# Kernel optimization log

Measured on AMD Instinct MI355X. Metric: run time of the kernel, lower is better.

Reference implementation:

```python
import jax, jax.numpy as jnp
import numpy as np

N_NODES = 100000
N_EDGES = 3200000
IN_DIM = 64
HID = 64


def setup_inputs() -> dict:
    key = jax.random.key(0)
    ks = jax.random.split(key, 12)
    x = jax.random.normal(ks[0], (N_NODES, IN_DIM), dtype=jnp.float32)
    edge_index = jax.random.randint(ks[1], (2, N_EDGES), 0, N_NODES, dtype=jnp.int64)
    tau = jax.random.uniform(ks[2], (N_NODES, 1), dtype=jnp.float32)
    d1 = IN_DIM + 1  # augmented feature dim
    s1 = 1.0 / np.sqrt(d1)
    s2 = 1.0 / np.sqrt(HID)
    # SAGEConv: out = lin_l(mean_aggr) + lin_r(x); bias lives in lin_l. Weights stored [in, out].
    W1l = jax.random.uniform(ks[3], (d1, HID), jnp.float32, -s1, s1)
    b1l = jax.random.uniform(ks[4], (HID,), jnp.float32, -s1, s1)
    W1r = jax.random.uniform(ks[5], (d1, HID), jnp.float32, -s1, s1)
    W2l = jax.random.uniform(ks[6], (HID, HID), jnp.float32, -s2, s2)
    b2l = jax.random.uniform(ks[7], (HID,), jnp.float32, -s2, s2)
    W2r = jax.random.uniform(ks[8], (HID, HID), jnp.float32, -s2, s2)
    Wfc = jax.random.uniform(ks[9], (HID, 1), jnp.float32, -s2, s2)
    bfc = jax.random.uniform(ks[10], (1,), jnp.float32, -s2, s2)
    return {"x": x, "edge_index": edge_index, "tau": tau,
            "W1l": W1l, "b1l": b1l, "W1r": W1r,
            "W2l": W2l, "b2l": b2l, "W2r": W2r,
            "Wfc": Wfc, "bfc": bfc}


def _sage_conv(x, src, dst, Wl, bl, Wr, n_nodes):
    # mean aggregation of source-node features onto target nodes
    summed = jax.ops.segment_sum(x[src], dst, num_segments=n_nodes)  # [N, d]
    deg = jax.ops.segment_sum(jnp.ones(src.shape[0], x.dtype), dst, num_segments=n_nodes)
    mean = summed / jnp.maximum(deg, 1.0)[:, None]
    return mean @ Wl + bl + x @ Wr


def reference(x, edge_index, tau, W1l, b1l, W1r, W2l, b2l, W2r, Wfc, bfc):
    src, dst = edge_index[0], edge_index[1]
    n = x.shape[0]
    h = jnp.concatenate([x, tau], axis=1)  # augment_features: append tau column
    h = jax.nn.relu(_sage_conv(h, src, dst, W1l, b1l, W1r, n))
    h = jax.nn.relu(_sage_conv(h, src, dst, W2l, b2l, W2r, n))
    return h @ Wfc + bfc  # [N, 1]
```

## Files before the change

kernel.cpp:

```cpp
#include <hip/hip_runtime.h>
#include <hip/hip_bf16.h>
#include <hip/hip_fp16.h>
#include <hip/hip_fp8.h>


#define BSH 7
#define NBKT 782
#define NBLK 256
#define CAP 6144
#define ABLK 512

typedef _Float16 half8 __attribute__((ext_vector_type(8)));
typedef float floatx4 __attribute__((ext_vector_type(4)));
typedef float floatx2 __attribute__((ext_vector_type(2)));

#if __has_builtin(__builtin_amdgcn_cvt_pk_f32_fp8)
__device__ __forceinline__ float2 f8x2_to_f2(unsigned short v) {
    floatx2 r = __builtin_amdgcn_cvt_pk_f32_fp8((int)(unsigned)v, false);
    return make_float2(r.x, r.y);
}
#else
__device__ __forceinline__ float2 f8x2_to_f2(unsigned short v) {
    __half2_raw r = __hip_cvt_fp8x2_to_halfraw2((__hip_fp8x2_storage_t)v, __HIP_E4M3);
    return __half22float2(*(__half2*)&r);
}
#endif

#if __has_builtin(__builtin_amdgcn_cvt_pk_fp8_f32)
__device__ __forceinline__ unsigned f4_to_f8x4(float a, float b, float c, float d) {
    int lo = __builtin_amdgcn_cvt_pk_fp8_f32(a, b, 0, false);
    return (unsigned)__builtin_amdgcn_cvt_pk_fp8_f32(c, d, lo, true);
}
__device__ __forceinline__ unsigned char f_to_f8(float a) {
    return (unsigned char)(__builtin_amdgcn_cvt_pk_fp8_f32(a, a, 0, false) & 0xFF);
}
#else
__device__ __forceinline__ unsigned f4_to_f8x4(float a, float b, float c, float d) {
    unsigned lo = (unsigned)__hip_cvt_float2_to_fp8x2(make_float2(a, b), __HIP_SATFINITE, __HIP_E4M3);
    unsigned hi = (unsigned)__hip_cvt_float2_to_fp8x2(make_float2(c, d), __HIP_SATFINITE, __HIP_E4M3);
    return lo | (hi << 16);
}
__device__ __forceinline__ unsigned char f_to_f8(float a) {
    return (unsigned char)__hip_cvt_float_to_fp8(a, __HIP_SATFINITE, __HIP_E4M3);
}
#endif

__global__ __launch_bounds__(256) void k_histprep(
    const int* __restrict__ dst, int* __restrict__ histT, int E,
    const float* __restrict__ x, __half* __restrict__ xh,
    unsigned char* __restrict__ xf8, int n4,
    const float* __restrict__ W1l, const float* __restrict__ W1r,
    const float* __restrict__ W2l, const float* __restrict__ W2r,
    __half* __restrict__ wbuf1, __half* __restrict__ wbuf2) {
    if (blockIdx.x < NBLK) {
        __shared__ int h[NBKT];
        for (int i = threadIdx.x; i < NBKT; i += 256) h[i] = 0;
        __syncthreads();
        int per = (E + NBLK - 1) / NBLK;
        int lo = blockIdx.x * per;
        int hi = lo + per; if (hi > E) hi = E;
        for (int e = lo + threadIdx.x; e < hi; e += 256)
            atomicAdd(&h[dst[e] >> BSH], 1);
        __syncthreads();
        for (int k = threadIdx.x; k < NBKT; k += 256)
            histT[k * NBLK + blockIdx.x] = h[k];
    } else if (blockIdx.x < NBLK + 9) {
        int idx = (blockIdx.x - NBLK) * 256 + threadIdx.x;
        if (idx < 1280) {
            int lane = idx & 63;
            int nt = (idx >> 6) & 3;
            int kstep = idx >> 8;
            int col = nt * 16 + (lane & 15);
            int kbase = kstep * 32 + (lane >> 4) * 8;
#pragma unroll
            for (int j = 0; j < 8; ++j) {
                int k = kbase + j;
                float v;
                if (k < 64)        v = W1l[k * 64 + col];
                else if (k < 128)  v = W1r[(k - 64) * 64 + col];
                else if (k == 128) v = W1l[64 * 64 + col];
                else if (k == 129) v = W1r[64 * 64 + col];
                else v = 0.f;
                wbuf1[(size_t)idx * 8 + j] = __float2half(v);
            }
        } else if (idx < 1280 + 1024) {
            int i2 = idx - 1280;
            int lane = i2 & 63;
            int nt = (i2 >> 6) & 3;
            int kstep = i2 >> 8;
            int col = nt * 16 + (lane & 15);
            int kbase = kstep * 32 + (lane >> 4) * 8;
#pragma unroll
            for (int j = 0; j < 8; ++j) {
                int k = kbase + j;
                float v = (k < 64) ? W2l[k * 64 + col] : W2r[(k - 64) * 64 + col];
                wbuf2[(size_t)i2 * 8 + j] = __float2half(v);
            }
        }
    } else {
        int i = (blockIdx.x - NBLK - 9) * 256 + threadIdx.x;
        if (i < n4) {
            float4 v = ((const float4*)x)[i];
            ((__half2*)xh)[2 * i]     = __floats2half2_rn(v.x, v.y);
            ((__half2*)xh)[2 * i + 1] = __floats2half2_rn(v.z, v.w);
            ((unsigned*)xf8)[i] = f4_to_f8x4(v.x, v.y, v.z, v.w);
        }
    }
}


__global__ __launch_bounds__(NBLK) void k_scanblk(int* __restrict__ histT,
                                                  int* __restrict__ btot) {
    __shared__ int s[NBLK];
    int k = blockIdx.x, t = threadIdx.x;
    int v = histT[k * NBLK + t];
    s[t] = v;
    __syncthreads();
    for (int off = 1; off < NBLK; off <<= 1) {
        int u = (t >= off) ? s[t - off] : 0;
        __syncthreads();
        s[t] += u;
        __syncthreads();
    }
    histT[k * NBLK + t] = s[t] - v;
    if (t == NBLK - 1) btot[k] = s[t];
}

__global__ __launch_bounds__(1024) void k_scanbkt(const int* __restrict__ btot,
                                                  int* __restrict__ bstart) {
    __shared__ int s[1024];
    int t = threadIdx.x;
    int v = (t < NBKT) ? btot[t] : 0;
    s[t] = v;
    __syncthreads();
    for (int off = 1; off < 1024; off <<= 1) {
        int u = (t >= off) ? s[t - off] : 0;
        __syncthreads();
        s[t] += u;
        __syncthreads();
    }
    if (t < NBKT) bstart[t] = s[t] - v;
    if (t == NBKT - 1) bstart[NBKT] = s[t];
}

__global__ __launch_bounds__(256) void k_scatter(const int* __restrict__ src,
                                                 const int* __restrict__ dst,
                                                 const int* __restrict__ histT,
                                                 const int* __restrict__ bstart,
                                                 int* __restrict__ binned, int E) {
    __shared__ int cur[NBKT];
    int b = blockIdx.x;
    for (int k = threadIdx.x; k < NBKT; k += 256)
        cur[k] = bstart[k] + histT[k * NBLK + b];
    __syncthreads();
    int per = (E + NBLK - 1) / NBLK;
    int lo = b * per;
    int hi = lo + per; if (hi > E) hi = E;
    for (int e = lo + threadIdx.x; e < hi; e += 256) {
        int d = dst[e], s = src[e];
        int pos = atomicAdd(&cur[d >> BSH], 1);
        binned[pos] = (s << BSH) | (d & ((1 << BSH) - 1));
    }
}


__global__ __launch_bounds__(ABLK) void k_aggrb1(
    const int* __restrict__ binned, const int* __restrict__ bstart,
    const unsigned char* __restrict__ xf8, const float* __restrict__ tau,
    __half* __restrict__ zm1, __half* __restrict__ mt1, int N) {
    __shared__ int cidx[CAP];
    __shared__ int cnt[128], s[128], cur[128];
    int k = blockIdx.x, t = threadIdx.x;
    int lo = bstart[k], hi = bstart[k + 1];
    if (t < 128) cnt[t] = 0;
    __syncthreads();
    for (int e = lo + t; e < hi; e += ABLK)
        atomicAdd(&cnt[binned[e] & 127], 1);
    __syncthreads();
    if (t < 128) s[t] = cnt[t];
    __syncthreads();
    for (int off = 1; off < 128; off <<= 1) {
        int u = 0;
        if (t < 128 && t >= off) u = s[t - off];
        __syncthreads();
        if (t < 128) s[t] += u;
        __syncthreads();
    }
    if (t < 128) cur[t] = s[t] - cnt[t];
    __syncthreads();
    for (int e = lo + t; e < hi; e += ABLK) {
        int p = binned[e];
        int pos = atomicAdd(&cur[p & 127], 1);
        if (pos < CAP) cidx[pos] = p >> BSH;
    }
    __syncthreads();

    int lane = t & 63;
    int halfid = lane >> 5;
    int c = lane & 31;
    unsigned cb = (unsigned)(c << 1);
    const char* xb = (const char*)xf8;

    for (int p = (t >> 6); p < 64; p += (ABLK / 64)) {
        int ld = (p << 1) + halfid;
        int node = (k << BSH) + ld;
        int d = cnt[ld];
        int startL = cur[ld] - d;
        int dother = __shfl_xor(d, 32, 64);
        float2 A0 = {0.f, 0.f}, A1 = A0, A2 = A0, A3 = A0;
        float sumtau = 0.f;
        for (int base = 0; base < d || base < dother; base += 32) {
            int n = d - base;
            n = (n < 0) ? 0 : (n > 32 ? 32 : n);
            int nmax = max(n, __shfl_xor(n, 32, 64));
            int sidx = 0;
            if (c < n) {
                int ii = startL + base + c;
                if (ii >= CAP) ii = 0;
                sidx = cidx[ii];
                sumtau += tau[sidx];
            }
            int j = 0;
            for (; j + 4 <= nmax; j += 4) {
                int i0 = __builtin_amdgcn_ds_bpermute((halfid * 32 + j + 0) << 2, sidx);
                int i1 = __builtin_amdgcn_ds_bpermute((halfid * 32 + j + 1) << 2, sidx);
                int i2 = __builtin_amdgcn_ds_bpermute((halfid * 32 + j + 2) << 2, sidx);
                int i3 = __builtin_amdgcn_ds_bpermute((halfid * 32 + j + 3) << 2, sidx);
                unsigned short r0 = *(const unsigned short*)(xb + (((unsigned)i0 << 6) + cb));
                unsigned short r1 = *(const unsigned short*)(xb + (((unsigned)i1 << 6) + cb));
                unsigned short r2 = *(const unsigned short*)(xb + (((unsigned)i2 << 6) + cb));
                unsigned short r3 = *(const unsigned short*)(xb + (((unsigned)i3 << 6) + cb));
                float2 v0 = f8x2_to_f2(r0);
                float2 v1 = f8x2_to_f2(r1);
                float2 v2 = f8x2_to_f2(r2);
                float2 v3 = f8x2_to_f2(r3);
                if (j + 0 < n) { A0.x += v0.x; A0.y += v0.y; }
                if (j + 1 < n) { A1.x += v1.x; A1.y += v1.y; }
                if (j + 2 < n) { A2.x += v2.x; A2.y += v2.y; }
                if (j + 3 < n) { A3.x += v3.x; A3.y += v3.y; }
            }
            for (; j < nmax; ++j) {
                int i0 = __builtin_amdgcn_ds_bpermute((halfid * 32 + j) << 2, sidx);
                unsigned short r0 = *(const unsigned short*)(xb + (((unsigned)i0 << 6) + cb));
                float2 v0 = f8x2_to_f2(r0);
                if (j < n) { A0.x += v0.x; A0.y += v0.y; }
            }
        }
        float2 A;
        A.x = (A0.x + A1.x) + (A2.x + A3.x);
        A.y = (A0.y + A1.y) + (A2.y + A3.y);
#pragma unroll
        for (int off = 16; off > 0; off >>= 1) sumtau += __shfl_xor(sumtau, off, 64);

        float inv = 1.f / fmaxf((float)d, 1.f);
        if (node < N) {
            ((__half2*)(zm1 + (size_t)node * 64))[c] =
                __floats2half2_rn(A.x * inv, A.y * inv);
            if (c == 0) mt1[node] = __float2half(sumtau * inv);
        }
    }
}

__global__ __launch_bounds__(ABLK) void k_aggrb2(
    const int* __restrict__ binned, const int* __restrict__ bstart,
    const unsigned char* __restrict__ h1f8, __half* __restrict__ zm2, int N) {
    __shared__ int cidx[CAP];
    __shared__ int cnt[128], s[128], cur[128];
    int k = blockIdx.x, t = threadIdx.x;
    int lo = bstart[k], hi = bstart[k + 1];
    if (t < 128) cnt[t] = 0;
    __syncthreads();
    for (int e = lo + t; e < hi; e += ABLK)
        atomicAdd(&cnt[binned[e] & 127], 1);
    __syncthreads();
    if (t < 128) s[t] = cnt[t];
    __syncthreads();
    for (int off = 1; off < 128; off <<= 1) {
        int u = 0;
        if (t < 128 && t >= off) u = s[t - off];
        __syncthreads();
        if (t < 128) s[t] += u;
        __syncthreads();
    }
    if (t < 128) cur[t] = s[t] - cnt[t];
    __syncthreads();
    for (int e = lo + t; e < hi; e += ABLK) {
        int p = binned[e];
        int pos = atomicAdd(&cur[p & 127], 1);
        if (pos < CAP) cidx[pos] = p >> BSH;
    }
    __syncthreads();

    int lane = t & 63;
    int halfid = lane >> 5;
    int c = lane & 31;
    unsigned cb = (unsigned)(c << 1);
    const char* hb = (const char*)h1f8;

    for (int p = (t >> 6); p < 64; p += (ABLK / 64)) {
        int ld = (p << 1) + halfid;
        int node = (k << BSH) + ld;
        int d = cnt[ld];
        int startL = cur[ld] - d;
        int dother = __shfl_xor(d, 32, 64);
        float2 A0 = {0.f, 0.f}, A1 = A0, A2 = A0, A3 = A0;
        for (int base = 0; base < d || base < dother; base += 32) {
            int n = d - base;
            n = (n < 0) ? 0 : (n > 32 ? 32 : n);
            int nmax = max(n, __shfl_xor(n, 32, 64));
            int sidx = 0;
            if (c < n) {
                int ii = startL + base + c;
                if (ii >= CAP) ii = 0;
                sidx = cidx[ii];
            }
            int j = 0;
            for (; j + 4 <= nmax; j += 4) {
                int i0 = __builtin_amdgcn_ds_bpermute((halfid * 32 + j + 0) << 2, sidx);
                int i1 = __builtin_amdgcn_ds_bpermute((halfid * 32 + j + 1) << 2, sidx);
                int i2 = __builtin_amdgcn_ds_bpermute((halfid * 32 + j + 2) << 2, sidx);
                int i3 = __builtin_amdgcn_ds_bpermute((halfid * 32 + j + 3) << 2, sidx);
                unsigned short r0 = *(const unsigned short*)(hb + (((unsigned)i0 << 6) + cb));
                unsigned short r1 = *(const unsigned short*)(hb + (((unsigned)i1 << 6) + cb));
                unsigned short r2 = *(const unsigned short*)(hb + (((unsigned)i2 << 6) + cb));
                unsigned short r3 = *(const unsigned short*)(hb + (((unsigned)i3 << 6) + cb));
                float2 v0 = f8x2_to_f2(r0);
                float2 v1 = f8x2_to_f2(r1);
                float2 v2 = f8x2_to_f2(r2);
                float2 v3 = f8x2_to_f2(r3);
                if (j + 0 < n) { A0.x += v0.x; A0.y += v0.y; }
                if (j + 1 < n) { A1.x += v1.x; A1.y += v1.y; }
                if (j + 2 < n) { A2.x += v2.x; A2.y += v2.y; }
                if (j + 3 < n) { A3.x += v3.x; A3.y += v3.y; }
            }
            for (; j < nmax; ++j) {
                int i0 = __builtin_amdgcn_ds_bpermute((halfid * 32 + j) << 2, sidx);
                unsigned short r0 = *(const unsigned short*)(hb + (((unsigned)i0 << 6) + cb));
                float2 v0 = f8x2_to_f2(r0);
                if (j < n) { A0.x += v0.x; A0.y += v0.y; }
            }
        }
        float2 A;
        A.x = (A0.x + A1.x) + (A2.x + A3.x);
        A.y = (A0.y + A1.y) + (A2.y + A3.y);
        float inv = 1.f / fmaxf((float)d, 1.f);
        if (node < N)
            ((__half2*)(zm2 + (size_t)node * 64))[c] =
                __floats2half2_rn(A.x * inv, A.y * inv);
    }
}


__global__ __launch_bounds__(256) void k_gemm1(
    const __half* __restrict__ zm1, const __half* __restrict__ mt1,
    const __half* __restrict__ xh, const float* __restrict__ tau,
    const __half* __restrict__ wbuf1, const float* __restrict__ b1l,
    __half* __restrict__ h1, unsigned char* __restrict__ h1f8, int ntiles) {
    int tile = blockIdx.x * 4 + (threadIdx.x >> 6);
    if (tile >= ntiles) return;
    int lane = threadIdx.x & 63;
    int sub = lane & 15;
    int quad = lane >> 4;
    int row = tile * 16 + sub;

    floatx4 acc0 = {0.f, 0.f, 0.f, 0.f};
    floatx4 acc1 = {0.f, 0.f, 0.f, 0.f};
    floatx4 acc2 = {0.f, 0.f, 0.f, 0.f};
    floatx4 acc3 = {0.f, 0.f, 0.f, 0.f};

    const _Float16* zrow = (const _Float16*)zm1 + (size_t)row * 64 + quad * 8;
    const _Float16* xrow = (const _Float16*)xh + (size_t)row * 64 + quad * 8;
    const _Float16* wb = (const _Float16*)wbuf1 + (size_t)lane * 8;

    half8 amat[5];
    amat[0] = *(const half8*)(zrow);
    amat[1] = *(const half8*)(zrow + 32);
    amat[2] = *(const half8*)(xrow);
    amat[3] = *(const half8*)(xrow + 32);
    half8 a4 = {0, 0, 0, 0, 0, 0, 0, 0};
    if (quad == 0) {
        a4[0] = ((const _Float16*)mt1)[row];
        a4[1] = (_Float16)tau[row];
    }
    amat[4] = a4;

#pragma unroll
    for (int ks = 0; ks < 5; ++ks) {
        half8 a = amat[ks];
        half8 b0 = *(const half8*)(wb + (size_t)(ks * 4 + 0) * 512);
        half8 b1 = *(const half8*)(wb + (size_t)(ks * 4 + 1) * 512);
        half8 b2 = *(const half8*)(wb + (size_t)(ks * 4 + 2) * 512);
        half8 b3 = *(const half8*)(wb + (size_t)(ks * 4 + 3) * 512);
        acc0 = __builtin_amdgcn_mfma_f32_16x16x32_f16(a, b0, acc0, 0, 0, 0);
        acc1 = __builtin_amdgcn_mfma_f32_16x16x32_f16(a, b1, acc1, 0, 0, 0);
        acc2 = __builtin_amdgcn_mfma_f32_16x16x32_f16(a, b2, acc2, 0, 0, 0);
        acc3 = __builtin_amdgcn_mfma_f32_16x16x32_f16(a, b3, acc3, 0, 0, 0);
    }
    float bv0 = b1l[sub], bv1 = b1l[16 + sub], bv2 = b1l[32 + sub], bv3 = b1l[48 + sub];
#pragma unroll
    for (int reg = 0; reg < 4; ++reg) {
        int r = quad * 4 + reg;
        float v0 = fmaxf(acc0[reg] + bv0, 0.f);
        float v1 = fmaxf(acc1[reg] + bv1, 0.f);
        float v2 = fmaxf(acc2[reg] + bv2, 0.f);
        float v3 = fmaxf(acc3[reg] + bv3, 0.f);
        __half* orow = h1 + (size_t)(tile * 16 + r) * 64;
        orow[sub]      = __float2half(v0);
        orow[16 + sub] = __float2half(v1);
        orow[32 + sub] = __float2half(v2);
        orow[48 + sub] = __float2half(v3);
        unsigned char* orow8 = h1f8 + (size_t)(tile * 16 + r) * 64;
        orow8[sub]      = f_to_f8(v0);
        orow8[16 + sub] = f_to_f8(v1);
        orow8[32 + sub] = f_to_f8(v2);
        orow8[48 + sub] = f_to_f8(v3);
    }
}

__global__ __launch_bounds__(256) void k_gemm2(
    const __half* __restrict__ zm2, const __half* __restrict__ h1,
    const __half* __restrict__ wbuf2, const float* __restrict__ b2l,
    const float* __restrict__ Wfc, const float* __restrict__ bfc,
    float* __restrict__ out, int ntiles) {
    int tile = blockIdx.x * 4 + (threadIdx.x >> 6);
    if (tile >= ntiles) return;
    int lane = threadIdx.x & 63;
    int sub = lane & 15;
    int quad = lane >> 4;
    int row = tile * 16 + sub;

    floatx4 acc0 = {0.f, 0.f, 0.f, 0.f};
    floatx4 acc1 = {0.f, 0.f, 0.f, 0.f};
    floatx4 acc2 = {0.f, 0.f, 0.f, 0.f};
    floatx4 acc3 = {0.f, 0.f, 0.f, 0.f};

    const _Float16* zrow = (const _Float16*)zm2 + (size_t)row * 64 + quad * 8;
    const _Float16* hrow = (const _Float16*)h1 + (size_t)row * 64 + quad * 8;
    const _Float16* wb = (const _Float16*)wbuf2 + (size_t)lane * 8;

    half8 amat[4];
    amat[0] = *(const half8*)(zrow);
    amat[1] = *(const half8*)(zrow + 32);
    amat[2] = *(const half8*)(hrow);
    amat[3] = *(const half8*)(hrow + 32);

#pragma unroll
    for (int ks = 0; ks < 4; ++ks) {
        half8 a = amat[ks];
        half8 b0 = *(const half8*)(wb + (size_t)(ks * 4 + 0) * 512);
        half8 b1 = *(const half8*)(wb + (size_t)(ks * 4 + 1) * 512);
        half8 b2 = *(const half8*)(wb + (size_t)(ks * 4 + 2) * 512);
        half8 b3 = *(const half8*)(wb + (size_t)(ks * 4 + 3) * 512);
        acc0 = __builtin_amdgcn_mfma_f32_16x16x32_f16(a, b0, acc0, 0, 0, 0);
        acc1 = __builtin_amdgcn_mfma_f32_16x16x32_f16(a, b1, acc1, 0, 0, 0);
        acc2 = __builtin_amdgcn_mfma_f32_16x16x32_f16(a, b2, acc2, 0, 0, 0);
        acc3 = __builtin_amdgcn_mfma_f32_16x16x32_f16(a, b3, acc3, 0, 0, 0);
    }
    float bb0 = b2l[sub], bb1 = b2l[16 + sub], bb2 = b2l[32 + sub], bb3 = b2l[48 + sub];
    float wv0 = Wfc[sub], wv1 = Wfc[16 + sub], wv2 = Wfc[32 + sub], wv3 = Wfc[48 + sub];
    float p[4];
#pragma unroll
    for (int reg = 0; reg < 4; ++reg) {
        p[reg] = fmaxf(acc0[reg] + bb0, 0.f) * wv0
               + fmaxf(acc1[reg] + bb1, 0.f) * wv1
               + fmaxf(acc2[reg] + bb2, 0.f) * wv2
               + fmaxf(acc3[reg] + bb3, 0.f) * wv3;
    }
#pragma unroll
    for (int m = 1; m <= 8; m <<= 1) {
#pragma unroll
        for (int reg = 0; reg < 4; ++reg) p[reg] += __shfl_xor(p[reg], m, 64);
    }
    if (sub == 0) {
        float b0 = bfc[0];
#pragma unroll
        for (int reg = 0; reg < 4; ++reg)
            out[tile * 16 + quad * 4 + reg] = p[reg] + b0;
    }
}

extern "C" void kernel_launch(void* const* d_in, const int* in_sizes, int n_in,
                              void* d_out, int out_size, void* d_ws, size_t ws_size,
                              hipStream_t stream) {
    const float* x   = (const float*)d_in[0];
    const int*   ei  = (const int*)d_in[1];
    const float* tau = (const float*)d_in[2];
    const float* W1l = (const float*)d_in[3];
    const float* b1l = (const float*)d_in[4];
    const float* W1r = (const float*)d_in[5];
    const float* W2l = (const float*)d_in[6];
    const float* b2l = (const float*)d_in[7];
    const float* W2r = (const float*)d_in[8];
    const float* Wfc = (const float*)d_in[9];
    const float* bfc = (const float*)d_in[10];
    float* out = (float*)d_out;

    const int N = in_sizes[0] / 64;
    const int E = in_sizes[1] / 2;
    const int* src = ei;
    const int* dst = ei + E;

    char* w = (char*)d_ws;
    auto take = [&](size_t b) { char* p = w; w += (b + 255) & ~(size_t)255; return p; };
    int*           histT  = (int*)take((size_t)NBKT * NBLK * 4);
    int*           btot   = (int*)take((size_t)NBKT * 4);
    int*           bstart = (int*)take((size_t)(NBKT + 1) * 4);
    int*           binned = (int*)take((size_t)E * 4);
    __half*        xh     = (__half*)take((size_t)N * 64 * 2);
    unsigned char* xf8    = (unsigned char*)take((size_t)N * 64);
    __half*        h1     = (__half*)take((size_t)N * 64 * 2);
    unsigned char* h1f8   = (unsigned char*)take((size_t)N * 64);
    __half*        zm1    = (__half*)take((size_t)N * 64 * 2);
    __half*        mt1    = (__half*)take((size_t)N * 2);
    __half*        zm2    = (__half*)take((size_t)N * 64 * 2);
    __half*        wbuf1  = (__half*)take(1280 * 8 * 2);
    __half*        wbuf2  = (__half*)take(1024 * 8 * 2);

    int n4 = N * 16;
    int hpblocks = NBLK + 9 + (n4 + 255) / 256;
    int ntiles = N / 16;
    int gblocks = (ntiles + 3) / 4;

    k_histprep<<<hpblocks, 256, 0, stream>>>(dst, histT, E, x, xh, xf8, n4,
                                             W1l, W1r, W2l, W2r, wbuf1, wbuf2);
    k_scanblk <<<NBKT, NBLK, 0, stream>>>(histT, btot);
    k_scanbkt <<<1, 1024, 0, stream>>>(btot, bstart);
    k_scatter <<<NBLK, 256, 0, stream>>>(src, dst, histT, bstart, binned, E);
    k_aggrb1  <<<NBKT, ABLK, 0, stream>>>(binned, bstart, xf8, tau, zm1, mt1, N);
    k_gemm1   <<<gblocks, 256, 0, stream>>>(zm1, mt1, xh, tau, wbuf1, b1l, h1, h1f8, ntiles);
    k_aggrb2  <<<NBKT, ABLK, 0, stream>>>(binned, bstart, h1f8, zm2, N);
    k_gemm2   <<<gblocks, 256, 0, stream>>>(zm2, h1, wbuf2, b2l, Wfc, bfc, out, ntiles);
}
```

Measured before the change: 305.5 us.

## Replace global bucket sort with per-block local bucketing and segmented gather

```diff
diff --git a/kernel.cpp b/kernel.cpp
--- a/kernel.cpp
+++ b/kernel.cpp
@@ -7,6 +7,7 @@
 #define BSH 7
 #define NBKT 782
 #define NBLK 256
+#define PER 12500
 #define CAP 6144
 #define ABLK 512
 
@@ -56,14 +57,13 @@
         __shared__ int h[NBKT];
         for (int i = threadIdx.x; i < NBKT; i += 256) h[i] = 0;
         __syncthreads();
-        int per = (E + NBLK - 1) / NBLK;
-        int lo = blockIdx.x * per;
-        int hi = lo + per; if (hi > E) hi = E;
+        int lo = blockIdx.x * PER;
+        int hi = lo + PER; if (hi > E) hi = E;
         for (int e = lo + threadIdx.x; e < hi; e += 256)
             atomicAdd(&h[dst[e] >> BSH], 1);
         __syncthreads();
         for (int k = threadIdx.x; k < NBKT; k += 256)
-            histT[k * NBLK + blockIdx.x] = h[k];
+            histT[(size_t)blockIdx.x * NBKT + k] = h[k];
     } else if (blockIdx.x < NBLK + 9) {
         int idx = (blockIdx.x - NBLK) * 256 + threadIdx.x;
         if (idx < 1280) {
@@ -108,29 +108,10 @@
     }
 }
 
-
-__global__ __launch_bounds__(NBLK) void k_scanblk(int* __restrict__ histT,
-                                                  int* __restrict__ btot) {
-    __shared__ int s[NBLK];
-    int k = blockIdx.x, t = threadIdx.x;
-    int v = histT[k * NBLK + t];
-    s[t] = v;
-    __syncthreads();
-    for (int off = 1; off < NBLK; off <<= 1) {
-        int u = (t >= off) ? s[t - off] : 0;
-        __syncthreads();
-        s[t] += u;
-        __syncthreads();
-    }
-    histT[k * NBLK + t] = s[t] - v;
-    if (t == NBLK - 1) btot[k] = s[t];
-}
-
-__global__ __launch_bounds__(1024) void k_scanbkt(const int* __restrict__ btot,
-                                                  int* __restrict__ bstart) {
+__global__ __launch_bounds__(1024) void k_scanrow(int* __restrict__ histT) {
     __shared__ int s[1024];
-    int t = threadIdx.x;
-    int v = (t < NBKT) ? btot[t] : 0;
+    int b = blockIdx.x, t = threadIdx.x;
+    int v = (t < NBKT) ? histT[(size_t)b * NBKT + t] : 0;
     s[t] = v;
     __syncthreads();
     for (int off = 1; off < 1024; off <<= 1) {
@@ -139,43 +120,50 @@
         s[t] += u;
         __syncthreads();
     }
-    if (t < NBKT) bstart[t] = s[t] - v;
-    if (t == NBKT - 1) bstart[NBKT] = s[t];
+    if (t < NBKT) histT[(size_t)b * NBKT + t] = s[t] - v;
 }
 
 __global__ __launch_bounds__(256) void k_scatter(const int* __restrict__ src,
                                                  const int* __restrict__ dst,
                                                  const int* __restrict__ histT,
-                                                 const int* __restrict__ bstart,
                                                  int* __restrict__ binned, int E) {
     __shared__ int cur[NBKT];
     int b = blockIdx.x;
+    int base = b * PER;
     for (int k = threadIdx.x; k < NBKT; k += 256)
-        cur[k] = bstart[k] + histT[k * NBLK + b];
-    __syncthreads();
-    int per = (E + NBLK - 1) / NBLK;
-    int lo = b * per;
-    int hi = lo + per; if (hi > E) hi = E;
-    for (int e = lo + threadIdx.x; e < hi; e += 256) {
+        cur[k] = histT[(size_t)b * NBKT + k];
+    __syncthreads();
+    int hi = base + PER; if (hi > E) hi = E;
+    for (int e = base + threadIdx.x; e < hi; e += 256) {
         int d = dst[e], s = src[e];
-        int pos = atomicAdd(&cur[d >> BSH], 1);
+        int pos = base + atomicAdd(&cur[d >> BSH], 1);
         binned[pos] = (s << BSH) | (d & ((1 << BSH) - 1));
     }
 }
 
 
 __global__ __launch_bounds__(ABLK) void k_aggrb1(
-    const int* __restrict__ binned, const int* __restrict__ bstart,
+    const int* __restrict__ binned, const int* __restrict__ histT,
     const unsigned char* __restrict__ xf8, const float* __restrict__ tau,
-    __half* __restrict__ zm1, __half* __restrict__ mt1, int N) {
+    __half* __restrict__ zm1, __half* __restrict__ mt1, int E, int N) {
     __shared__ int cidx[CAP];
+    __shared__ int rst[NBLK], rlen[NBLK];
     __shared__ int cnt[128], s[128], cur[128];
     int k = blockIdx.x, t = threadIdx.x;
-    int lo = bstart[k], hi = bstart[k + 1];
+    for (int b = t; b < NBLK; b += ABLK) {
+        int off = histT[(size_t)b * NBKT + k];
+        int blen = E - b * PER; if (blen > PER) blen = PER;
+        int nxt = (k + 1 < NBKT) ? histT[(size_t)b * NBKT + k + 1] : blen;
+        rst[b] = b * PER + off;
+        rlen[b] = nxt - off;
+    }
     if (t < 128) cnt[t] = 0;
     __syncthreads();
-    for (int e = lo + t; e < hi; e += ABLK)
-        atomicAdd(&cnt[binned[e] & 127], 1);
+    for (int b = t; b < NBLK; b += ABLK) {
+        int st = rst[b], ln = rlen[b];
+        for (int i = 0; i < ln; ++i)
+            atomicAdd(&cnt[binned[st + i] & 127], 1);
+    }
     __syncthreads();
     if (t < 128) s[t] = cnt[t];
     __syncthreads();
@@ -188,10 +176,13 @@
     }
     if (t < 128) cur[t] = s[t] - cnt[t];
     __syncthreads();
-    for (int e = lo + t; e < hi; e += ABLK) {
-        int p = binned[e];
-        int pos = atomicAdd(&cur[p & 127], 1);
-        if (pos < CAP) cidx[pos] = p >> BSH;
+    for (int b = t; b < NBLK; b += ABLK) {
+        int st = rst[b], ln = rlen[b];
+        for (int i = 0; i < ln; ++i) {
+            int p = binned[st + i];
+            int pos = atomicAdd(&cur[p & 127], 1);
+            if (pos < CAP) cidx[pos] = p >> BSH;
+        }
     }
     __syncthreads();
 
@@ -262,16 +253,27 @@
 }
 
 __global__ __launch_bounds__(ABLK) void k_aggrb2(
-    const int* __restrict__ binned, const int* __restrict__ bstart,
-    const unsigned char* __restrict__ h1f8, __half* __restrict__ zm2, int N) {
+    const int* __restrict__ binned, const int* __restrict__ histT,
+    const unsigned char* __restrict__ h1f8, __half* __restrict__ zm2,
+    int E, int N) {
     __shared__ int cidx[CAP];
+    __shared__ int rst[NBLK], rlen[NBLK];
     __shared__ int cnt[128], s[128], cur[128];
     int k = blockIdx.x, t = threadIdx.x;
-    int lo = bstart[k], hi = bstart[k + 1];
+    for (int b = t; b < NBLK; b += ABLK) {
+        int off = histT[(size_t)b * NBKT + k];
+        int blen = E - b * PER; if (blen > PER) blen = PER;
+        int nxt = (k + 1 < NBKT) ? histT[(size_t)b * NBKT + k + 1] : blen;
+        rst[b] = b * PER + off;
+        rlen[b] = nxt - off;
+    }
     if (t < 128) cnt[t] = 0;
     __syncthreads();
-    for (int e = lo + t; e < hi; e += ABLK)
-        atomicAdd(&cnt[binned[e] & 127], 1);
+    for (int b = t; b < NBLK; b += ABLK) {
+        int st = rst[b], ln = rlen[b];
+        for (int i = 0; i < ln; ++i)
+            atomicAdd(&cnt[binned[st + i] & 127], 1);
+    }
     __syncthreads();
     if (t < 128) s[t] = cnt[t];
     __syncthreads();
@@ -284,10 +286,13 @@
     }
     if (t < 128) cur[t] = s[t] - cnt[t];
     __syncthreads();
-    for (int e = lo + t; e < hi; e += ABLK) {
-        int p = binned[e];
-        int pos = atomicAdd(&cur[p & 127], 1);
-        if (pos < CAP) cidx[pos] = p >> BSH;
+    for (int b = t; b < NBLK; b += ABLK) {
+        int st = rst[b], ln = rlen[b];
+        for (int i = 0; i < ln; ++i) {
+            int p = binned[st + i];
+            int pos = atomicAdd(&cur[p & 127], 1);
+            if (pos < CAP) cidx[pos] = p >> BSH;
+        }
     }
     __syncthreads();
 
@@ -502,9 +507,7 @@
 
     char* w = (char*)d_ws;
     auto take = [&](size_t b) { char* p = w; w += (b + 255) & ~(size_t)255; return p; };
-    int*           histT  = (int*)take((size_t)NBKT * NBLK * 4);
-    int*           btot   = (int*)take((size_t)NBKT * 4);
-    int*           bstart = (int*)take((size_t)(NBKT + 1) * 4);
+    int*           histT  = (int*)take((size_t)NBLK * NBKT * 4);
     int*           binned = (int*)take((size_t)E * 4);
     __half*        xh     = (__half*)take((size_t)N * 64 * 2);
     unsigned char* xf8    = (unsigned char*)take((size_t)N * 64);
@@ -523,11 +526,10 @@
 
     k_histprep<<<hpblocks, 256, 0, stream>>>(dst, histT, E, x, xh, xf8, n4,
                                              W1l, W1r, W2l, W2r, wbuf1, wbuf2);
-    k_scanblk <<<NBKT, NBLK, 0, stream>>>(histT, btot);
-    k_scanbkt <<<1, 1024, 0, stream>>>(btot, bstart);
-    k_scatter <<<NBLK, 256, 0, stream>>>(src, dst, histT, bstart, binned, E);
-    k_aggrb1  <<<NBKT, ABLK, 0, stream>>>(binned, bstart, xf8, tau, zm1, mt1, N);
+    k_scanrow <<<NBLK, 1024, 0, stream>>>(histT);
+    k_scatter <<<NBLK, 256, 0, stream>>>(src, dst, histT, binned, E);
+    k_aggrb1  <<<NBKT, ABLK, 0, stream>>>(binned, histT, xf8, tau, zm1, mt1, E, N);
     k_gemm1   <<<gblocks, 256, 0, stream>>>(zm1, mt1, xh, tau, wbuf1, b1l, h1, h1f8, ntiles);
-    k_aggrb2  <<<NBKT, ABLK, 0, stream>>>(binned, bstart, h1f8, zm2, N);
+    k_aggrb2  <<<NBKT, ABLK, 0, stream>>>(binned, histT, h1f8, zm2, E, N);
     k_gemm2   <<<gblocks, 256, 0, stream>>>(zm2, h1, wbuf2, b2l, Wfc, bfc, out, ntiles);
 }
```

New measurement: 329.7 us. +7.9%, slower.

## Stage scatter through shared-memory local sort for coalesced binned writes

Applied to the files above, without the earlier changes.

```diff
diff --git a/kernel.cpp b/kernel.cpp
--- a/kernel.cpp
+++ b/kernel.cpp
@@ -7,6 +7,7 @@
 #define BSH 7
 #define NBKT 782
 #define NBLK 256
+#define PER 12500
 #define CAP 6144
 #define ABLK 512
 
@@ -56,9 +57,8 @@
         __shared__ int h[NBKT];
         for (int i = threadIdx.x; i < NBKT; i += 256) h[i] = 0;
         __syncthreads();
-        int per = (E + NBLK - 1) / NBLK;
-        int lo = blockIdx.x * per;
-        int hi = lo + per; if (hi > E) hi = E;
+        int lo = blockIdx.x * PER;
+        int hi = lo + PER; if (hi > E) hi = E;
         for (int e = lo + threadIdx.x; e < hi; e += 256)
             atomicAdd(&h[dst[e] >> BSH], 1);
         __syncthreads();
@@ -148,18 +148,64 @@
                                                  const int* __restrict__ histT,
                                                  const int* __restrict__ bstart,
                                                  int* __restrict__ binned, int E) {
+    __shared__ int sorted[PER];
+    __shared__ int lstart[NBKT + 1];
     __shared__ int cur[NBKT];
-    int b = blockIdx.x;
-    for (int k = threadIdx.x; k < NBKT; k += 256)
-        cur[k] = bstart[k] + histT[k * NBLK + b];
-    __syncthreads();
-    int per = (E + NBLK - 1) / NBLK;
-    int lo = b * per;
-    int hi = lo + per; if (hi > E) hi = E;
-    for (int e = lo + threadIdx.x; e < hi; e += 256) {
+    __shared__ int gst[NBKT];
+    __shared__ int tsum[256];
+    int b = blockIdx.x, t = threadIdx.x;
+    int base = b * PER;
+    int blen = E - base; if (blen > PER) blen = PER;
+
+    for (int k = t; k < NBKT; k += 256) lstart[k] = 0;
+    __syncthreads();
+    for (int e = base + t; e < base + blen; e += 256)
+        atomicAdd(&lstart[dst[e] >> BSH], 1);
+    __syncthreads();
+    int c0 = 0;
+    int i0 = t * 4;
+#pragma unroll
+    for (int j = 0; j < 4; ++j)
+        if (i0 + j < NBKT) c0 += lstart[i0 + j];
+    tsum[t] = c0;
+    __syncthreads();
+    for (int off = 1; off < 256; off <<= 1) {
+        int u = (t >= off) ? tsum[t - off] : 0;
+        __syncthreads();
+        tsum[t] += u;
+        __syncthreads();
+    }
+    int running = tsum[t] - c0;
+    __syncthreads();
+#pragma unroll
+    for (int j = 0; j < 4; ++j) {
+        int i = i0 + j;
+        if (i < NBKT) {
+            int v = lstart[i];
+            lstart[i] = running;
+            running += v;
+        }
+    }
+    __syncthreads();
+    if (t == 0) lstart[NBKT] = blen;
+    for (int k = t; k < NBKT; k += 256) {
+        cur[k] = lstart[k];
+        gst[k] = bstart[k] + histT[k * NBLK + b];
+    }
+    __syncthreads();
+    for (int e = base + t; e < base + blen; e += 256) {
         int d = dst[e], s = src[e];
         int pos = atomicAdd(&cur[d >> BSH], 1);
-        binned[pos] = (s << BSH) | (d & ((1 << BSH) - 1));
+        sorted[pos] = (s << BSH) | (d & ((1 << BSH) - 1));
+    }
+    __syncthreads();
+    int wid = t >> 6, lane = t & 63;
+    for (int k = wid; k < NBKT; k += 4) {
+        int st = lstart[k];
+        int ln = lstart[k + 1] - st;
+        int gd = gst[k];
+        for (int i = lane; i < ln; i += 64)
+            binned[gd + i] = sorted[st + i];
     }
 }
 
```

Result: slower. 318.4 us (+4.2%).
